# Kernel optimization log

Measured on AMD Instinct MI355X. Metric: run time of the kernel, lower is better.

## Reference

```python
import jax, jax.numpy as jnp
import numpy as np

DIM = 192; EXP = 2; QKB = 4
INNER = EXP * DIM          # 384
NH = INNER // QKB          # 96 heads
DH = QKB                   # 4 dims per head
Hs, Ws = 24, 24; S = Hs * Ws; B = 1; K = 3
EPS = 1e-6


def setup_inputs() -> dict:
    key = jax.random.key(0)
    ks = jax.random.split(key, 16)
    sm_up = (2.0 / (5.0 * DIM)) ** 0.5
    sm_dn = (2.0 / (5.0 * INNER)) ** 0.5
    def n(k, shape, s):
        return jax.random.normal(k, shape, jnp.float32) * s
    return {
        "x": jax.random.normal(ks[0], (B, S, DIM), jnp.float32),
        "d": jax.random.normal(ks[1], (B, S, DIM), jnp.float32),
        "ln_w": jnp.ones((DIM,), jnp.float32),
        "ln_b": jnp.zeros((DIM,), jnp.float32),
        "up_w": n(ks[2], (2 * INNER, DIM), sm_up),
        "up_b": jnp.zeros((2 * INNER,), jnp.float32),
        "dup_w": n(ks[3], (INNER, DIM), sm_up),
        "dup_b": jnp.zeros((INNER,), jnp.float32),
        "q_w": n(ks[4], (NH, DH, DH), sm_up), "q_b": jnp.zeros((INNER,), jnp.float32),
        "k_w": n(ks[5], (NH, DH, DH), sm_up), "k_b": jnp.zeros((INNER,), jnp.float32),
        "v_w": n(ks[6], (NH, DH, DH), sm_up), "v_b": jnp.zeros((INNER,), jnp.float32),
        "conv_w": n(ks[7], (INNER, K, K), 0.1), "conv_b": jnp.zeros((INNER,), jnp.float32),
        "ig_w": n(ks[8], (NH, 3 * INNER), 0.01),
        "ig_b": jax.random.normal(ks[9], (NH,), jnp.float32) * 0.1 - 3.0,
        "fg_w": jnp.zeros((NH, 3 * INNER), jnp.float32),
        "fg_b": jnp.linspace(3.0, 6.0, NH, dtype=jnp.float32),
        "onorm_w": jnp.ones((INNER,), jnp.float32),
        "skip": jnp.ones((INNER,), jnp.float32),
        "down_w": n(ks[10], (DIM, INNER), sm_dn),
        "down_b": jnp.zeros((DIM,), jnp.float32),
    }


def _headwise(x, w, b):
    # LinearHeadwiseExpand: block-diagonal linear, per-head DHxDH matrix
    Bx, Sx, _ = x.shape
    y = jnp.einsum('bsni,noi->bsno', x.reshape(Bx, Sx, NH, DH), w)
    return y.reshape(Bx, Sx, INNER) + b


def _mlstm(q, k, v, ig, fg, onorm_w):
    # parallel_stabilized_simple: q,k,v [B,NH,S,DH]; ig,fg [B,NH,S]
    Sq = q.shape[2]
    log_f = jax.nn.log_sigmoid(fg)                    # [B,NH,S]
    lfc = jnp.cumsum(log_f, axis=-1)                  # cumulative log forget
    logfm = lfc[..., :, None] - lfc[..., None, :]     # [B,NH,S,S]
    mask = jnp.tril(jnp.ones((Sq, Sq), dtype=bool))
    logD = jnp.where(mask, logfm + ig[..., None, :], -jnp.inf)
    maxD = jnp.max(logD, axis=-1, keepdims=True)      # [B,NH,S,1] stabilizer
    Dm = jnp.exp(logD - maxD)
    C = jnp.einsum('bnsd,bntd->bnst', q, k / (DH ** 0.5)) * Dm
    norm = jnp.maximum(jnp.abs(C.sum(-1, keepdims=True)), jnp.exp(-maxD))
    h = jnp.einsum('bnst,bntd->bnsd', C / (norm + EPS), v)
    # MultiHeadLayerNorm (group norm over DH per head, weight only)
    mu = h.mean(-1, keepdims=True)
    var = h.var(-1, keepdims=True)
    return (h - mu) / jnp.sqrt(var + 1e-5) * onorm_w.reshape(NH, DH)[None, :, None, :]


def _forward(x, d, ln_w, ln_b, up_w, up_b, dup_w, dup_b, q_w, q_b, k_w, k_b,
             v_w, v_b, conv_w, conv_b, ig_w, ig_b, fg_w, fg_b, onorm_w, skip,
             down_w, down_b):
    Bx, Sx, _ = x.shape
    # pre-norm LayerNorm
    mu = x.mean(-1, keepdims=True)
    var = x.var(-1, keepdims=True)
    xn = (x - mu) / jnp.sqrt(var + 1e-5) * ln_w + ln_b
    x_inner = xn @ up_w.T + up_b                      # [B,S,2*INNER]
    x_mlstm, z = jnp.split(x_inner, 2, axis=-1)
    d_mlstm = d @ dup_w.T + dup_b                     # dead code in original forward
    # depthwise 3x3 conv over the HxW token grid (SequenceConv2d, groups=INNER)
    kern = jnp.transpose(conv_w, (1, 2, 0))[:, :, None, :]   # HWIO
    xc = jax.lax.conv_general_dilated(
        x_mlstm.reshape(Bx, Hs, Ws, INNER), kern, (1, 1), 'SAME',
        dimension_numbers=('NHWC', 'HWIO', 'NHWC'),
        feature_group_count=INNER) + conv_b
    xa = jax.nn.silu(xc.reshape(Bx, Sx, INNER))
    q = _headwise(xa, q_w, q_b)
    k = _headwise(xa, k_w, k_b)
    v = _headwise(x_mlstm, v_w, v_b)
    gin = jnp.concatenate([q, k, v], axis=-1)         # [B,S,3*INNER]
    ig = (gin @ ig_w.T + ig_b).transpose(0, 2, 1)     # [B,NH,S]
    fg = (gin @ fg_w.T + fg_b).transpose(0, 2, 1)
    to_h = lambda t: t.reshape(Bx, Sx, NH, DH).transpose(0, 2, 1, 3)
    h = _mlstm(to_h(q), to_h(k), to_h(v), ig, fg, onorm_w)   # [B,NH,S,DH]
    h = h.transpose(0, 2, 1, 3).reshape(Bx, Sx, INNER)
    h = (h + skip * xa) * jax.nn.silu(z)
    return h @ down_w.T + down_b


def reference(x, d, ln_w, ln_b, up_w, up_b, dup_w, dup_b, q_w, q_b, k_w, k_b,
              v_w, v_b, conv_w, conv_b, ig_w, ig_b, fg_w, fg_b, onorm_w, skip,
              down_w, down_b):
    return _forward(x, d, ln_w, ln_b, up_w, up_b, dup_w, dup_b, q_w, q_b,
                    k_w, k_b, v_w, v_b, conv_w, conv_b, ig_w, ig_b, fg_w,
                    fg_b, onorm_w, skip, down_w, down_b)
```

## Files before the change

### kernel.cpp

```cpp
#include <hip/hip_runtime.h>
#include <math.h>

#define SEQ 576
#define DIM 192
#define INNER 384
#define NHEAD 96
#define HS 24
#define WSZ 24
#define GIN 1152
#define GKS 4

__global__ __launch_bounds__(256) void k_up(const float* __restrict__ x,
    const float* __restrict__ lnw, const float* __restrict__ lnb,
    const float* __restrict__ w, const float* __restrict__ b,
    float* __restrict__ out) {
  int m0 = blockIdx.x * 64, n0 = blockIdx.y * 32;
  __shared__ float As[DIM * 64];
  __shared__ float Bs[DIM * 32];
  __shared__ float mu[64], inv[64], ps[192];
  int t = threadIdx.x;
  for (int idx = t; idx < 64 * 48; idx += 256) {
    int r = idx / 48, k4 = idx % 48;
    float4 v = *(const float4*)&x[(m0 + r) * DIM + 4 * k4];
    int rw = r ^ (4 * (k4 & 15));
    As[(4 * k4 + 0) * 64 + rw] = v.x;
    As[(4 * k4 + 1) * 64 + rw] = v.y;
    As[(4 * k4 + 2) * 64 + rw] = v.z;
    As[(4 * k4 + 3) * 64 + rw] = v.w;
  }
  for (int idx = t; idx < 32 * 48; idx += 256) {
    int r = idx / 48, k4 = idx % 48;
    float4 v = *(const float4*)&w[(n0 + r) * DIM + 4 * k4];
    int rw = r ^ (4 * (k4 & 7));
    Bs[(4 * k4 + 0) * 32 + rw] = v.x;
    Bs[(4 * k4 + 1) * 32 + rw] = v.y;
    Bs[(4 * k4 + 2) * 32 + rw] = v.z;
    Bs[(4 * k4 + 3) * 32 + rw] = v.w;
  }
  __syncthreads();
  if (t < 192) {
    int r = t % 64, ph = t / 64;
    float s_ = 0.f;
    #pragma unroll 8
    for (int k = ph * 64; k < ph * 64 + 64; ++k)
      s_ += As[k * 64 + (r ^ (4 * ((k >> 2) & 15)))];
    ps[t] = s_;
  }
  __syncthreads();
  if (t < 64) mu[t] = (ps[t] + ps[64 + t] + ps[128 + t]) * (1.0f / DIM);
  __syncthreads();
  if (t < 192) {
    int r = t % 64, ph = t / 64;
    float m_ = mu[r], s_ = 0.f;
    #pragma unroll 8
    for (int k = ph * 64; k < ph * 64 + 64; ++k) {
      float d = As[k * 64 + (r ^ (4 * ((k >> 2) & 15)))] - m_;
      s_ += d * d;
    }
    ps[t] = s_;
  }
  __syncthreads();
  if (t < 64) inv[t] = rsqrtf((ps[t] + ps[64 + t] + ps[128 + t]) * (1.0f / DIM) + 1e-5f);
  __syncthreads();
  for (int idx = t; idx < 64 * DIM; idx += 256) {
    int k = idx >> 6, r0 = idx & 63;
    int m = r0 ^ (4 * ((k >> 2) & 15));
    As[idx] = (As[idx] - mu[m]) * inv[m] * lnw[k] + lnb[k];
  }
  __syncthreads();
  int gm = t >> 4, gn = t & 15;
  float acc[4][2];
  #pragma unroll
  for (int i = 0; i < 4; ++i)
    #pragma unroll
    for (int j = 0; j < 2; ++j) acc[i][j] = b[n0 + 2 * gn + j];
  #pragma unroll 4
  for (int kk = 0; kk < DIM; ++kk) {
    int mk = (kk >> 2) & 15, nk = 4 * ((kk >> 2) & 7);
    float4 a = *(const float4*)&As[kk * 64 + 4 * (gm ^ mk)];
    float2 bv = *(const float2*)&Bs[kk * 32 + ((2 * gn) ^ nk)];
    acc[0][0] += a.x * bv.x; acc[0][1] += a.x * bv.y;
    acc[1][0] += a.y * bv.x; acc[1][1] += a.y * bv.y;
    acc[2][0] += a.z * bv.x; acc[2][1] += a.z * bv.y;
    acc[3][0] += a.w * bv.x; acc[3][1] += a.w * bv.y;
  }
  #pragma unroll
  for (int i = 0; i < 4; ++i)
    *(float2*)&out[(m0 + 4 * gm + i) * (2 * INNER) + n0 + 2 * gn] =
        make_float2(acc[i][0], acc[i][1]);
}

__global__ __launch_bounds__(384) void k_cqkv(const float* __restrict__ xin,
    const float* __restrict__ cw, const float* __restrict__ cb,
    const float* __restrict__ qw, const float* __restrict__ qb,
    const float* __restrict__ kw, const float* __restrict__ kb,
    const float* __restrict__ vw, const float* __restrict__ vb,
    float* __restrict__ xa, float* __restrict__ ginT) {
  int s = blockIdx.x, t = threadIdx.x;
  int h = s / WSZ, wc = s % WSZ;
  __shared__ float xat[INNER], xmt[INNER];
  float acc = cb[t];
  #pragma unroll
  for (int kh = 0; kh < 3; ++kh) {
    int hh = h + kh - 1;
    if (hh < 0 || hh >= HS) continue;
    #pragma unroll
    for (int kw2 = 0; kw2 < 3; ++kw2) {
      int ww = wc + kw2 - 1;
      if (ww < 0 || ww >= WSZ) continue;
      acc += xin[(hh * WSZ + ww) * (2 * INNER) + t] * cw[t * 9 + kh * 3 + kw2];
    }
  }
  float sil = acc / (1.0f + __expf(-acc));
  xat[t] = sil;
  xa[s * INNER + t] = sil;
  xmt[t] = xin[s * (2 * INNER) + t];
  __syncthreads();
  int n = t >> 2, o = t & 3;
  const float* xah = xat + n * 4;
  const float* xmh = xmt + n * 4;
  float q = qb[t], k = kb[t], v = vb[t];
  #pragma unroll
  for (int i = 0; i < 4; ++i) {
    float xq = xah[i], xm = xmh[i];
    q += xq * qw[n * 16 + o * 4 + i];
    k += xq * kw[n * 16 + o * 4 + i];
    v += xm * vw[n * 16 + o * 4 + i];
  }
  ginT[t * SEQ + s]               = q;
  ginT[(INNER + t) * SEQ + s]     = k;
  ginT[(2 * INNER + t) * SEQ + s] = v;
}

#define GBK 288
__global__ __launch_bounds__(256) void k_gates(const float* __restrict__ ginT,
    const float* __restrict__ igw, const float* __restrict__ fgw,
    float* __restrict__ pig, float* __restrict__ pfg) {
  int bx = blockIdx.x, s0 = blockIdx.y * 64, ks = blockIdx.z;
  int k0 = ks * GBK;
  bool isig = bx < 3;
  int m0 = (isig ? bx : bx - 3) * 32;
  const float* wb = (isig ? igw : fgw) + m0 * GIN;
  __shared__ float Ws[GBK * 32];
  __shared__ float Gs[GBK * 64];
  int t = threadIdx.x;
  for (int idx = t; idx < 32 * 72; idx += 256) {
    int r = idx / 72, k4 = idx % 72;
    float4 v = *(const float4*)&wb[r * GIN + k0 + 4 * k4];
    int rw = r ^ (4 * (k4 & 7));
    Ws[(4 * k4 + 0) * 32 + rw] = v.x;
    Ws[(4 * k4 + 1) * 32 + rw] = v.y;
    Ws[(4 * k4 + 2) * 32 + rw] = v.z;
    Ws[(4 * k4 + 3) * 32 + rw] = v.w;
  }
  for (int idx = t; idx < GBK * 16; idx += 256) {
    int kk = idx / 16, s4 = idx % 16;
    *(float4*)&Gs[kk * 64 + 4 * s4] =
        *(const float4*)&ginT[(k0 + kk) * SEQ + s0 + 4 * s4];
  }
  __syncthreads();
  int gm = t >> 4, gn = t & 15;
  float acc[2][4] = {{0.f,0.f,0.f,0.f},{0.f,0.f,0.f,0.f}};
  #pragma unroll 4
  for (int kk = 0; kk < GBK; ++kk) {
    int nk = 4 * ((kk >> 2) & 7);
    float2 wv = *(const float2*)&Ws[kk * 32 + ((2 * gm) ^ nk)];
    float4 gv = *(const float4*)&Gs[kk * 64 + 4 * gn];
    acc[0][0] += wv.x * gv.x; acc[0][1] += wv.x * gv.y;
    acc[0][2] += wv.x * gv.z; acc[0][3] += wv.x * gv.w;
    acc[1][0] += wv.y * gv.x; acc[1][1] += wv.y * gv.y;
    acc[1][2] += wv.y * gv.z; acc[1][3] += wv.y * gv.w;
  }
  float* dstp = (isig ? pig : pfg) + ks * NHEAD * SEQ;
  #pragma unroll
  for (int i = 0; i < 2; ++i) {
    int mm = m0 + 2 * gm + i;
    *(float4*)&dstp[mm * SEQ + s0 + 4 * gn] =
        make_float4(acc[i][0], acc[i][1], acc[i][2], acc[i][3]);
  }
}

__global__ __launch_bounds__(576) void k_mlstm(const float* __restrict__ ginT,
    const float* __restrict__ pig, const float* __restrict__ pfg,
    const float* __restrict__ igb, const float* __restrict__ fgb,
    const float* __restrict__ onw, float* __restrict__ hout) {
  int n = blockIdx.x, hh = blockIdx.y, t = threadIdx.x;
  int cnt2 = 288 * (hh + 1);
  __shared__ float ksm[SEQ * 4], vsm[SEQ * 4], esm[SEQ];
  __shared__ float bufA[SEQ], bufB[SEQ], bufC[SEQ];
  const int H4 = NHEAD * SEQ;
  float ai = 0.f;
  if (t < cnt2) {
    float a0 = ginT[(INNER + n * 4 + 0) * SEQ + t] * 0.5f;
    float a1 = ginT[(INNER + n * 4 + 1) * SEQ + t] * 0.5f;
    float a2 = ginT[(INNER + n * 4 + 2) * SEQ + t] * 0.5f;
    float a3 = ginT[(INNER + n * 4 + 3) * SEQ + t] * 0.5f;
    *(float4*)&ksm[t * 4] = make_float4(a0, a1, a2, a3);
    float b0 = ginT[(2 * INNER + n * 4 + 0) * SEQ + t];
    float b1 = ginT[(2 * INNER + n * 4 + 1) * SEQ + t];
    float b2 = ginT[(2 * INNER + n * 4 + 2) * SEQ + t];
    float b3 = ginT[(2 * INNER + n * 4 + 3) * SEQ + t];
    *(float4*)&vsm[t * 4] = make_float4(b0, b1, b2, b3);
    int off = n * SEQ + t;
    ai = igb[n] + pig[off] + pig[off + H4] + pig[off + 2 * H4] + pig[off + 3 * H4];
    float af = fgb[n] + pfg[off] + pfg[off + H4] + pfg[off + 2 * H4] + pfg[off + 3 * H4];
    float lf = (af >= 0.f) ? -log1pf(expf(-af)) : (af - log1pf(expf(af)));
    bufA[t] = lf;
  }
  __syncthreads();
  float* src = bufA; float* dst = bufB;
  for (int o2 = 1; o2 < cnt2; o2 <<= 1) {
    if (t < cnt2) {
      float v = src[t];
      if (t >= o2) v += src[t - o2];
      dst[t] = v;
    }
    __syncthreads();
    float* tmp = src; src = dst; dst = tmp;
  }
  if (t < cnt2) {
    float e = ai - src[t];
    esm[t] = e;
    dst[t] = e;
  }
  __syncthreads();
  float* srcM = dst; float* dstM = bufC;
  for (int o2 = 1; o2 < cnt2; o2 <<= 1) {
    if (t < cnt2) {
      float v = srcM[t];
      if (t >= o2) v = fmaxf(v, srcM[t - o2]);
      dstM[t] = v;
    }
    __syncthreads();
    float* tmp = srcM; srcM = dstM; dstM = tmp;
  }
  int r = (t < 288) ? t : t - 288;
  int half = (t >= 288) ? 1 : 0;
  int s = 288 * hh + r;
  float pm = srcM[s];
  float mxv = src[s] + pm;
  float q0 = ginT[(n * 4 + 0) * SEQ + s];
  float q1 = ginT[(n * 4 + 1) * SEQ + s];
  float q2 = ginT[(n * 4 + 2) * SEQ + s];
  float q3 = ginT[(n * 4 + 3) * SEQ + s];
  int N = s + 1, nA = (N + 1) >> 1;
  int lo = half ? nA : 0, hi = half ? N : nA;
  float csum = 0.f, h0 = 0.f, h1 = 0.f, h2 = 0.f, h3 = 0.f;
  for (int tt = lo; tt < hi; ++tt) {
    float d = __expf(esm[tt] - pm);
    float c = (q0 * ksm[tt*4] + q1 * ksm[tt*4+1] + q2 * ksm[tt*4+2] + q3 * ksm[tt*4+3]) * d;
    csum += c;
    h0 += c * vsm[tt*4]; h1 += c * vsm[tt*4+1]; h2 += c * vsm[tt*4+2]; h3 += c * vsm[tt*4+3];
  }
  __syncthreads();
  if (half) {
    ksm[r * 5 + 0] = csum; ksm[r * 5 + 1] = h0; ksm[r * 5 + 2] = h1;
    ksm[r * 5 + 3] = h2;   ksm[r * 5 + 4] = h3;
  }
  __syncthreads();
  if (!half) {
    csum += ksm[r * 5 + 0];
    h0 += ksm[r * 5 + 1]; h1 += ksm[r * 5 + 2];
    h2 += ksm[r * 5 + 3]; h3 += ksm[r * 5 + 4];
    float norm = fmaxf(fabsf(csum), __expf(-mxv)) + 1e-6f;
    float rr = 1.0f / norm;
    h0 *= rr; h1 *= rr; h2 *= rr; h3 *= rr;
    float mu = (h0 + h1 + h2 + h3) * 0.25f;
    float d0 = h0 - mu, d1 = h1 - mu, d2 = h2 - mu, d3 = h3 - mu;
    float var = (d0 * d0 + d1 * d1 + d2 * d2 + d3 * d3) * 0.25f;
    float inv = rsqrtf(var + 1e-5f);
    *(float4*)&hout[s * INNER + n * 4] = make_float4(
        d0 * inv * onw[n * 4 + 0], d1 * inv * onw[n * 4 + 1],
        d2 * inv * onw[n * 4 + 2], d3 * inv * onw[n * 4 + 3]);
  }
}

#define KPA 388
__global__ __launch_bounds__(128) void k_down(const float* __restrict__ hmat,
    const float* __restrict__ xa, const float* __restrict__ xin,
    const float* __restrict__ skip, const float* __restrict__ dw,
    const float* __restrict__ db, float* __restrict__ out) {
  int m0 = blockIdx.x * 16, n0 = blockIdx.y * 32;
  __shared__ float As[16 * KPA];
  __shared__ float Bs[INNER * 32];
  int t = threadIdx.x;
  for (int idx = t; idx < 16 * 96; idx += 128) {
    int r = idx / 96, k4 = idx % 96;
    int s = m0 + r;
    float4 zv = *(const float4*)&xin[s * (2 * INNER) + INNER + 4 * k4];
    float4 hm = *(const float4*)&hmat[s * INNER + 4 * k4];
    float4 xv = *(const float4*)&xa[s * INNER + 4 * k4];
    float4 sk = *(const float4*)&skip[4 * k4];
    float z, sil;
    float4 o;
    z = zv.x; sil = z / (1.0f + __expf(-z)); o.x = (hm.x + sk.x * xv.x) * sil;
    z = zv.y; sil = z / (1.0f + __expf(-z)); o.y = (hm.y + sk.y * xv.y) * sil;
    z = zv.z; sil = z / (1.0f + __expf(-z)); o.z = (hm.z + sk.z * xv.z) * sil;
    z = zv.w; sil = z / (1.0f + __expf(-z)); o.w = (hm.w + sk.w * xv.w) * sil;
    *(float4*)&As[r * KPA + 4 * k4] = o;
  }
  for (int idx = t; idx < 32 * 96; idx += 128) {
    int r = idx / 96, k4 = idx % 96;
    float4 v = *(const float4*)&dw[(n0 + r) * INNER + 4 * k4];
    int rw = r ^ (4 * (k4 & 7));
    Bs[(4 * k4 + 0) * 32 + rw] = v.x;
    Bs[(4 * k4 + 1) * 32 + rw] = v.y;
    Bs[(4 * k4 + 2) * 32 + rw] = v.z;
    Bs[(4 * k4 + 3) * 32 + rw] = v.w;
  }
  __syncthreads();
  int gm = t >> 4, gn = t & 15;
  float acc[2][2];
  #pragma unroll
  for (int i = 0; i < 2; ++i)
    #pragma unroll
    for (int j = 0; j < 2; ++j) acc[i][j] = db[n0 + 2 * gn + j];
  #pragma unroll 4
  for (int kk = 0; kk < INNER; ++kk) {
    int nk = 4 * ((kk >> 2) & 7);
    float a0 = As[(2 * gm) * KPA + kk];
    float a1 = As[(2 * gm + 1) * KPA + kk];
    float2 bv = *(const float2*)&Bs[kk * 32 + ((2 * gn) ^ nk)];
    acc[0][0] += a0 * bv.x; acc[0][1] += a0 * bv.y;
    acc[1][0] += a1 * bv.x; acc[1][1] += a1 * bv.y;
  }
  #pragma unroll
  for (int i = 0; i < 2; ++i)
    *(float2*)&out[(m0 + 2 * gm + i) * DIM + n0 + 2 * gn] =
        make_float2(acc[i][0], acc[i][1]);
}

extern "C" void kernel_launch(void* const* d_in, const int* in_sizes, int n_in,
                              void* d_out, int out_size, void* d_ws, size_t ws_size,
                              hipStream_t stream) {
  const float* x      = (const float*)d_in[0];
  const float* ln_w   = (const float*)d_in[2];
  const float* ln_b   = (const float*)d_in[3];
  const float* up_w   = (const float*)d_in[4];
  const float* up_b   = (const float*)d_in[5];
  const float* q_w    = (const float*)d_in[8];
  const float* q_b    = (const float*)d_in[9];
  const float* k_w    = (const float*)d_in[10];
  const float* k_b    = (const float*)d_in[11];
  const float* v_w    = (const float*)d_in[12];
  const float* v_b    = (const float*)d_in[13];
  const float* conv_w = (const float*)d_in[14];
  const float* conv_b = (const float*)d_in[15];
  const float* ig_w   = (const float*)d_in[16];
  const float* ig_b   = (const float*)d_in[17];
  const float* fg_w   = (const float*)d_in[18];
  const float* fg_b   = (const float*)d_in[19];
  const float* onorm_w= (const float*)d_in[20];
  const float* skip   = (const float*)d_in[21];
  const float* down_w = (const float*)d_in[22];
  const float* down_b = (const float*)d_in[23];
  float* out = (float*)d_out;

  float* ws     = (float*)d_ws;
  float* xinner = ws;
  float* xa     = xinner + SEQ * 2 * INNER;
  float* ginT   = xa + SEQ * INNER;
  float* pig    = ginT + GIN * SEQ;
  float* pfg    = pig + GKS * NHEAD * SEQ;
  float* hbuf   = pfg + GKS * NHEAD * SEQ;

  k_up   <<<dim3(9, 24), 256, 0, stream>>>(x, ln_w, ln_b, up_w, up_b, xinner);
  k_cqkv <<<SEQ, 384, 0, stream>>>(xinner, conv_w, conv_b,
                                   q_w, q_b, k_w, k_b, v_w, v_b, xa, ginT);
  k_gates<<<dim3(6, 9, GKS), 256, 0, stream>>>(ginT, ig_w, fg_w, pig, pfg);
  k_mlstm<<<dim3(NHEAD, 2), 576, 0, stream>>>(ginT, pig, pfg, ig_b, fg_b, onorm_w, hbuf);
  k_down <<<dim3(36, 6), 128, 0, stream>>>(hbuf, xa, xinner, skip, down_w, down_b, out);
}
```

Before: 103.9 us.

## Use wave-shuffle scans and 4-row register tiling in mLSTM kernel

Replaces the shared-memory Hillis-Steele prefix sum and prefix max, each of which used about ten block-wide barriers, with a wave-level shuffle scan followed by a small cross-wave scan. The attention loop is restructured so each group of 8 threads owns 4 query rows and splits the key range into 8 chunks. This reuses each key/value load across 4 rows and balances work better than the old two-way half split, and the partial sums are combined with shuffle reductions. In exchange it adds per-row causal branches inside the inner loop and more registers per thread.

```diff
diff --git a/kernel.cpp b/kernel.cpp
--- a/kernel.cpp
+++ b/kernel.cpp
@@ -185,11 +185,15 @@
     const float* __restrict__ igb, const float* __restrict__ fgb,
     const float* __restrict__ onw, float* __restrict__ hout) {
   int n = blockIdx.x, hh = blockIdx.y, t = threadIdx.x;
-  int cnt2 = 288 * (hh + 1);
+  int base = 288 * hh;
+  int cnt2 = base + 288;
   __shared__ float ksm[SEQ * 4], vsm[SEQ * 4], esm[SEQ];
-  __shared__ float bufA[SEQ], bufB[SEQ], bufC[SEQ];
+  __shared__ float qsm[288 * 4];
+  __shared__ float lfcs[SEQ], pms[SEQ];
+  __shared__ float wsum[16], wmax[16];
   const int H4 = NHEAD * SEQ;
-  float ai = 0.f;
+  int lane = t & 63, w = t >> 6;
+  float ai = 0.f, lf = 0.f;
   if (t < cnt2) {
     float a0 = ginT[(INNER + n * 4 + 0) * SEQ + t] * 0.5f;
     float a1 = ginT[(INNER + n * 4 + 1) * SEQ + t] * 0.5f;
@@ -201,77 +205,124 @@
     float b2 = ginT[(2 * INNER + n * 4 + 2) * SEQ + t];
     float b3 = ginT[(2 * INNER + n * 4 + 3) * SEQ + t];
     *(float4*)&vsm[t * 4] = make_float4(b0, b1, b2, b3);
+    if (t >= base) {
+      int r = t - base;
+      qsm[r * 4 + 0] = ginT[(n * 4 + 0) * SEQ + t];
+      qsm[r * 4 + 1] = ginT[(n * 4 + 1) * SEQ + t];
+      qsm[r * 4 + 2] = ginT[(n * 4 + 2) * SEQ + t];
+      qsm[r * 4 + 3] = ginT[(n * 4 + 3) * SEQ + t];
+    }
     int off = n * SEQ + t;
     ai = igb[n] + pig[off] + pig[off + H4] + pig[off + 2 * H4] + pig[off + 3 * H4];
     float af = fgb[n] + pfg[off] + pfg[off + H4] + pfg[off + 2 * H4] + pfg[off + 3 * H4];
-    float lf = (af >= 0.f) ? -log1pf(expf(-af)) : (af - log1pf(expf(af)));
-    bufA[t] = lf;
-  }
-  __syncthreads();
-  float* src = bufA; float* dst = bufB;
-  for (int o2 = 1; o2 < cnt2; o2 <<= 1) {
-    if (t < cnt2) {
-      float v = src[t];
-      if (t >= o2) v += src[t - o2];
-      dst[t] = v;
-    }
-    __syncthreads();
-    float* tmp = src; src = dst; dst = tmp;
-  }
+    lf = (af >= 0.f) ? -log1pf(expf(-af)) : (af - log1pf(expf(af)));
+  }
+  float v = (t < cnt2) ? lf : 0.f;
+  #pragma unroll
+  for (int o2 = 1; o2 < 64; o2 <<= 1) {
+    float u = __shfl_up(v, o2);
+    if (lane >= o2) v += u;
+  }
+  if (lane == 63) wsum[w] = v;
+  __syncthreads();
+  if (t < 16) {
+    float sv = (t < 9) ? wsum[t] : 0.f;
+    #pragma unroll
+    for (int o2 = 1; o2 < 16; o2 <<= 1) {
+      float u = __shfl_up(sv, o2);
+      if (t >= o2) sv += u;
+    }
+    wsum[t] = sv;
+  }
+  __syncthreads();
+  float lfc = v + ((w > 0) ? wsum[w - 1] : 0.f);
+  float e = ai - lfc;
+  float m = (t < cnt2) ? e : -3.0e38f;
+  #pragma unroll
+  for (int o2 = 1; o2 < 64; o2 <<= 1) {
+    float u = __shfl_up(m, o2);
+    if (lane >= o2) m = fmaxf(m, u);
+  }
+  if (lane == 63) wmax[w] = m;
+  __syncthreads();
+  if (t < 16) {
+    float sv = (t < 9) ? wmax[t] : -3.0e38f;
+    #pragma unroll
+    for (int o2 = 1; o2 < 16; o2 <<= 1) {
+      float u = __shfl_up(sv, o2);
+      if (t >= o2) sv = fmaxf(sv, u);
+    }
+    wmax[t] = sv;
+  }
+  __syncthreads();
+  float pm = (w > 0) ? fmaxf(m, wmax[w - 1]) : m;
   if (t < cnt2) {
-    float e = ai - src[t];
     esm[t] = e;
-    dst[t] = e;
-  }
-  __syncthreads();
-  float* srcM = dst; float* dstM = bufC;
-  for (int o2 = 1; o2 < cnt2; o2 <<= 1) {
-    if (t < cnt2) {
-      float v = srcM[t];
-      if (t >= o2) v = fmaxf(v, srcM[t - o2]);
-      dstM[t] = v;
-    }
-    __syncthreads();
-    float* tmp = srcM; srcM = dstM; dstM = tmp;
-  }
-  int r = (t < 288) ? t : t - 288;
-  int half = (t >= 288) ? 1 : 0;
-  int s = 288 * hh + r;
-  float pm = srcM[s];
-  float mxv = src[s] + pm;
-  float q0 = ginT[(n * 4 + 0) * SEQ + s];
-  float q1 = ginT[(n * 4 + 1) * SEQ + s];
-  float q2 = ginT[(n * 4 + 2) * SEQ + s];
-  float q3 = ginT[(n * 4 + 3) * SEQ + s];
-  int N = s + 1, nA = (N + 1) >> 1;
-  int lo = half ? nA : 0, hi = half ? N : nA;
-  float csum = 0.f, h0 = 0.f, h1 = 0.f, h2 = 0.f, h3 = 0.f;
+    lfcs[t] = lfc;
+    pms[t] = pm;
+  }
+  __syncthreads();
+  int rq = t >> 3, cq = t & 7;
+  int s0 = base + 4 * rq;
+  int N = s0 + 4;
+  float pmv[4], qv[4][4];
+  #pragma unroll
+  for (int i = 0; i < 4; ++i) {
+    pmv[i] = pms[s0 + i];
+    *(float4*)&qv[i][0] = *(float4*)&qsm[(4 * rq + i) * 4];
+  }
+  int ch = (N + 7) >> 3;
+  int lo = cq * ch, hi = min(lo + ch, N);
+  float cs[4] = {0.f, 0.f, 0.f, 0.f};
+  float hv[4][4];
+  #pragma unroll
+  for (int i = 0; i < 4; ++i)
+    #pragma unroll
+    for (int j = 0; j < 4; ++j) hv[i][j] = 0.f;
   for (int tt = lo; tt < hi; ++tt) {
-    float d = __expf(esm[tt] - pm);
-    float c = (q0 * ksm[tt*4] + q1 * ksm[tt*4+1] + q2 * ksm[tt*4+2] + q3 * ksm[tt*4+3]) * d;
-    csum += c;
-    h0 += c * vsm[tt*4]; h1 += c * vsm[tt*4+1]; h2 += c * vsm[tt*4+2]; h3 += c * vsm[tt*4+3];
-  }
-  __syncthreads();
-  if (half) {
-    ksm[r * 5 + 0] = csum; ksm[r * 5 + 1] = h0; ksm[r * 5 + 2] = h1;
-    ksm[r * 5 + 3] = h2;   ksm[r * 5 + 4] = h3;
-  }
-  __syncthreads();
-  if (!half) {
-    csum += ksm[r * 5 + 0];
-    h0 += ksm[r * 5 + 1]; h1 += ksm[r * 5 + 2];
-    h2 += ksm[r * 5 + 3]; h3 += ksm[r * 5 + 4];
-    float norm = fmaxf(fabsf(csum), __expf(-mxv)) + 1e-6f;
-    float rr = 1.0f / norm;
-    h0 *= rr; h1 *= rr; h2 *= rr; h3 *= rr;
-    float mu = (h0 + h1 + h2 + h3) * 0.25f;
-    float d0 = h0 - mu, d1 = h1 - mu, d2 = h2 - mu, d3 = h3 - mu;
-    float var = (d0 * d0 + d1 * d1 + d2 * d2 + d3 * d3) * 0.25f;
-    float inv = rsqrtf(var + 1e-5f);
-    *(float4*)&hout[s * INNER + n * 4] = make_float4(
-        d0 * inv * onw[n * 4 + 0], d1 * inv * onw[n * 4 + 1],
-        d2 * inv * onw[n * 4 + 2], d3 * inv * onw[n * 4 + 3]);
+    float e3 = esm[tt];
+    float4 kv = *(const float4*)&ksm[tt * 4];
+    float4 vv = *(const float4*)&vsm[tt * 4];
+    #pragma unroll
+    for (int i = 0; i < 4; ++i) {
+      if (tt <= s0 + i) {
+        float d = __expf(e3 - pmv[i]);
+        float c = (qv[i][0] * kv.x + qv[i][1] * kv.y +
+                   qv[i][2] * kv.z + qv[i][3] * kv.w) * d;
+        cs[i] += c;
+        hv[i][0] += c * vv.x; hv[i][1] += c * vv.y;
+        hv[i][2] += c * vv.z; hv[i][3] += c * vv.w;
+      }
+    }
+  }
+  #pragma unroll
+  for (int o2 = 4; o2 > 0; o2 >>= 1) {
+    #pragma unroll
+    for (int i = 0; i < 4; ++i) {
+      cs[i] += __shfl_down(cs[i], o2);
+      hv[i][0] += __shfl_down(hv[i][0], o2);
+      hv[i][1] += __shfl_down(hv[i][1], o2);
+      hv[i][2] += __shfl_down(hv[i][2], o2);
+      hv[i][3] += __shfl_down(hv[i][3], o2);
+    }
+  }
+  if (cq == 0) {
+    #pragma unroll
+    for (int i = 0; i < 4; ++i) {
+      int s = s0 + i;
+      float mxv = lfcs[s] + pmv[i];
+      float norm = fmaxf(fabsf(cs[i]), __expf(-mxv)) + 1e-6f;
+      float rr = 1.0f / norm;
+      float h0 = hv[i][0] * rr, h1 = hv[i][1] * rr;
+      float h2 = hv[i][2] * rr, h3 = hv[i][3] * rr;
+      float mu = (h0 + h1 + h2 + h3) * 0.25f;
+      float d0 = h0 - mu, d1 = h1 - mu, d2 = h2 - mu, d3 = h3 - mu;
+      float var = (d0 * d0 + d1 * d1 + d2 * d2 + d3 * d3) * 0.25f;
+      float inv = rsqrtf(var + 1e-5f);
+      *(float4*)&hout[s * INNER + n * 4] = make_float4(
+          d0 * inv * onw[n * 4 + 0], d1 * inv * onw[n * 4 + 1],
+          d2 * inv * onw[n * 4 + 2], d3 * inv * onw[n * 4 + 3]);
+    }
   }
 }
 
```

New measurement: 101.5 us. 2.3% less time.
